# Kernel optimization log

Hardware: AMD Instinct MI355X
Metric: run time of the kernel (lower is better)

## Reference

```python
import jax, jax.numpy as jnp
import numpy as np
import math

RCR = 5.2
NUM_SPECIES = 7
AEV_DIM = 1008
WIDTHS = [1008, 256, 192, 160]


def setup_inputs() -> dict:
    key = jax.random.key(0)
    ks = jax.random.split(key, 12)
    B, N = 1, 2048
    species = jax.random.randint(ks[0], (B, N), 0, NUM_SPECIES, dtype=jnp.int64 if jax.config.read('jax_enable_x64') else jnp.int32)
    coordinates = jax.random.uniform(ks[1], (B, N, 3), dtype=jnp.float32) * 6.0
    EtaR = jnp.array([16.0], dtype=jnp.float32)
    ShfR = jnp.array([0.9 + 0.18 * x for x in range(16)], dtype=jnp.float32)
    s = 0.05
    W0 = jax.random.normal(ks[2], (NUM_SPECIES, WIDTHS[1], WIDTHS[0]), jnp.float32) * s
    b0 = jax.random.normal(ks[3], (NUM_SPECIES, WIDTHS[1]), jnp.float32) * s
    W1 = jax.random.normal(ks[4], (NUM_SPECIES, WIDTHS[2], WIDTHS[1]), jnp.float32) * s
    b1 = jax.random.normal(ks[5], (NUM_SPECIES, WIDTHS[2]), jnp.float32) * s
    W2 = jax.random.normal(ks[6], (NUM_SPECIES, WIDTHS[3], WIDTHS[2]), jnp.float32) * s
    b2 = jax.random.normal(ks[7], (NUM_SPECIES, WIDTHS[3]), jnp.float32) * s
    Wf = jax.random.normal(ks[8], (NUM_SPECIES, 1, WIDTHS[3]), jnp.float32) * s
    bf = jax.random.normal(ks[9], (NUM_SPECIES, 1), jnp.float32) * s
    return {'species': species, 'coordinates': coordinates, 'EtaR': EtaR, 'ShfR': ShfR,
            'W0': W0, 'b0': b0, 'W1': W1, 'b1': b1, 'W2': W2, 'b2': b2, 'Wf': Wf, 'bf': bf}


def _celu(x, alpha=0.1):
    return jnp.maximum(x, 0.0) + jnp.minimum(0.0, alpha * jnp.expm1(x / alpha))


def _aev(species, coordinates, EtaR, ShfR):
    B, N = species.shape
    diff = coordinates[:, :, None, :] - coordinates[:, None, :, :]  # [B,N,N,3]
    dsq = jnp.sum(diff * diff, axis=-1)
    safe = jnp.where(dsq > 0, dsq, 1.0)
    dist = jnp.sqrt(safe)  # [B,N,N], diag is a dummy 1.0
    mask = (dsq > 0) & (dist <= RCR)
    fc = (0.5 * jnp.cos(math.pi * dist / RCR) + 0.5) * mask.astype(jnp.float32)
    onehot = jax.nn.one_hot(species, NUM_SPECIES, dtype=jnp.float32)  # [B,N,S]
    core = jnp.exp(-EtaR[0] * (dist[..., None] - ShfR) ** 2)  # [B,N,N,R]
    weighted = core * fc[..., None]
    # sum over neighbor j, grouped by neighbor species s (species-major concat order)
    radial = jnp.einsum('bijr,bjs->bisr', weighted, onehot)  # [B,N,S,R]
    radial = radial.reshape(B, N, NUM_SPECIES * ShfR.shape[0])
    pad = AEV_DIM - radial.shape[-1]
    return jnp.pad(radial, ((0, 0), (0, 0), (0, pad)))


def reference(species, coordinates, EtaR, ShfR, W0, b0, W1, b1, W2, b2, Wf, bf):
    aev = _aev(species, coordinates, EtaR, ShfR)  # [B,N,1008]
    # run all 7 element nets on every atom (matches the module's redundant-compute semantics)
    h = _celu(jnp.einsum('soh,bnh->sbno', W0, aev) + b0[:, None, None, :])
    h = _celu(jnp.einsum('soh,sbnh->sbno', W1, h) + b1[:, None, None, :])
    h = _celu(jnp.einsum('soh,sbnh->sbno', W2, h) + b2[:, None, None, :])
    e = jnp.einsum('soh,sbnh->sbno', Wf, h) + bf[:, None, None, :]  # [S,B,N,1]
    onehot = jax.nn.one_hot(species, NUM_SPECIES, dtype=jnp.float32)  # [B,N,S]
    total = jnp.einsum('sbn,bns->', e[..., 0], onehot)
    return total.reshape(1)
```

## Files before the change

kernel.cpp:

```cpp
#include <hip/hip_runtime.h>

#define N_ATOMS 2048
#define NSPEC 7
#define NR 16
#define NFEAT 112
#define RCR_F 5.2f
#define H0 256
#define H1 192
#define H2 160
#define W0_PITCH 1008
#define TILE 8
#define NTILES (N_ATOMS / TILE)

#define WS_SEG     0
#define WS_SCOORD  16384
#define WS_AEV     65536

__device__ __forceinline__ float celu01(float x) {
    return x > 0.f ? x : 0.1f * (__expf(x * 10.f) - 1.f);
}

__global__ __launch_bounds__(256) void sort_kernel(const int* __restrict__ species,
                                                   const float* __restrict__ coords,
                                                   int* __restrict__ seg,
                                                   float4* __restrict__ scoord,
                                                   float* __restrict__ out) {
    __shared__ int cnt[NSPEC];
    __shared__ int cur[NSPEC];
    int t = threadIdx.x;
    if (t < NSPEC) cnt[t] = 0;
    __syncthreads();
    for (int a = t; a < N_ATOMS; a += 256) atomicAdd(&cnt[species[a]], 1);
    __syncthreads();
    if (t == 0) {
        int run = 0;
        for (int s = 0; s < NSPEC; s++) { seg[s] = run; cur[s] = run; run += cnt[s]; }
        seg[NSPEC] = run;
        out[0] = 0.0f;
    }
    __syncthreads();
    for (int a = t; a < N_ATOMS; a += 256) {
        int sp = species[a];
        int pos = atomicAdd(&cur[sp], 1);
        scoord[pos] = make_float4(coords[3*a], coords[3*a+1], coords[3*a+2], 0.f);
    }
}

__global__ __launch_bounds__(256) void aev_kernel(const float4* __restrict__ scoord,
                                                  const int* __restrict__ seg,
                                                  const float* __restrict__ ShfR,
                                                  const float* __restrict__ EtaR,
                                                  float* __restrict__ aev) {
    int s = blockIdx.y;
    int p = blockIdx.x * 4 + (threadIdx.x >> 6);
    int lane = threadIdx.x & 63;

    float4 ci = scoord[p];
    float eta = EtaR[0];
    float shf[NR];
#pragma unroll
    for (int r = 0; r < NR; r++) shf[r] = ShfR[r];
    float acc[NR];
#pragma unroll
    for (int r = 0; r < NR; r++) acc[r] = 0.f;

    int kbeg = seg[s] + lane;
    int kend = seg[s + 1];
    const float rc2 = RCR_F * RCR_F;
    const float cosk = 3.14159265358979f / RCR_F;

    for (int k = kbeg; k < kend; k += 64) {
        float4 cj = scoord[k];
        float dx = ci.x - cj.x, dy = ci.y - cj.y, dz = ci.z - cj.z;
        float dsq = dx*dx + dy*dy + dz*dz;
        bool valid = (dsq > 0.f) && (dsq <= rc2);
        float d = sqrtf(dsq);
        float fc = 0.5f * __cosf(d * cosk) + 0.5f;
        fc = valid ? fc : 0.f;
#pragma unroll
        for (int r = 0; r < NR; r++) {
            float u = d - shf[r];
            acc[r] = fmaf(__expf(-eta * u * u), fc, acc[r]);
        }
    }
#pragma unroll
    for (int r = 0; r < NR; r++) {
        float v = acc[r];
        v += __shfl_xor(v, 1);
        v += __shfl_xor(v, 2);
        v += __shfl_xor(v, 4);
        v += __shfl_xor(v, 8);
        v += __shfl_xor(v, 16);
        v += __shfl_xor(v, 32);
        acc[r] = v;
    }
    if (lane == 0) {
        float* dst = aev + (size_t)p * NFEAT + s * NR;
#pragma unroll
        for (int r = 0; r < NR; r += 4)
            *(float4*)(dst + r) = make_float4(acc[r], acc[r+1], acc[r+2], acc[r+3]);
    }
}

__global__ __launch_bounds__(512) void mlp_kernel(const float* __restrict__ aev,
                                                  const int* __restrict__ seg,
                                                  const float* __restrict__ W0,
                                                  const float* __restrict__ b0,
                                                  const float* __restrict__ W1,
                                                  const float* __restrict__ b1,
                                                  const float* __restrict__ W2,
                                                  const float* __restrict__ b2,
                                                  const float* __restrict__ Wf,
                                                  const float* __restrict__ bf,
                                                  float* __restrict__ out) {
    __shared__ float aevs[TILE][NFEAT];
    __shared__ float h0s[TILE][H0];
    __shared__ float h1s[TILE][H1];
    __shared__ float bsum;

    int s = blockIdx.y;
    int segend = seg[s + 1];
    int base = seg[s] + blockIdx.x * TILE;
    if (base >= segend) return;
    int n_act = min(TILE, segend - base);

    int t = threadIdx.x;
    if (t == 0) bsum = 0.f;

    {
        float4* dst = (float4*)&aevs[0][0];
        const float4* src = (const float4*)(aev + (size_t)base * NFEAT);
        int nfl4 = min(TILE * (NFEAT / 4), (N_ATOMS - base) * (NFEAT / 4));
        for (int j = t; j < TILE * (NFEAT / 4); j += 512)
            dst[j] = (j < nfl4) ? src[j] : make_float4(0.f, 0.f, 0.f, 0.f);
    }
    __syncthreads();

    int o = t >> 1, ks = t & 1;

    {
        const float* Wr = W0 + (size_t)(s * H0 + o) * W0_PITCH + ks * 4;
        float bias = b0[s * H0 + o];
        float acc[TILE];
#pragma unroll
        for (int q = 0; q < TILE; q++) acc[q] = 0.f;
#pragma unroll 7
        for (int i = 0; i < NFEAT / 8; i++) {
            float4 w = *(const float4*)(Wr + i * 8);
#pragma unroll
            for (int q = 0; q < TILE; q++) {
                float4 a = *(const float4*)(&aevs[q][i * 8 + ks * 4]);
                acc[q] += w.x*a.x + w.y*a.y + w.z*a.z + w.w*a.w;
            }
        }
#pragma unroll
        for (int q = 0; q < TILE; q++) {
            float v = acc[q];
            v += __shfl_xor(v, 1);
            if (ks == 0) h0s[q][o] = celu01(v + bias);
        }
    }
    __syncthreads();

    if (o < H1) {
        const float* Wr = W1 + (size_t)(s * H1 + o) * H0 + ks * 4;
        float bias = b1[s * H1 + o];
        float acc[TILE];
#pragma unroll
        for (int q = 0; q < TILE; q++) acc[q] = 0.f;
#pragma unroll 4
        for (int i = 0; i < H0 / 8; i++) {
            float4 w = *(const float4*)(Wr + i * 8);
#pragma unroll
            for (int q = 0; q < TILE; q++) {
                float4 a = *(const float4*)(&h0s[q][i * 8 + ks * 4]);
                acc[q] += w.x*a.x + w.y*a.y + w.z*a.z + w.w*a.w;
            }
        }
#pragma unroll
        for (int q = 0; q < TILE; q++) {
            float v = acc[q];
            v += __shfl_xor(v, 1);
            if (ks == 0) h1s[q][o] = celu01(v + bias);
        }
    }
    __syncthreads();

    float contrib = 0.f;
    if (o < H2) {
        const float* Wr = W2 + (size_t)(s * H2 + o) * H1 + ks * 4;
        float bias = b2[s * H2 + o];
        float wf = Wf[s * H2 + o];
        float acc[TILE];
#pragma unroll
        for (int q = 0; q < TILE; q++) acc[q] = 0.f;
#pragma unroll 4
        for (int i = 0; i < H1 / 8; i++) {
            float4 w = *(const float4*)(Wr + i * 8);
#pragma unroll
            for (int q = 0; q < TILE; q++) {
                float4 a = *(const float4*)(&h1s[q][i * 8 + ks * 4]);
                acc[q] += w.x*a.x + w.y*a.y + w.z*a.z + w.w*a.w;
            }
        }
#pragma unroll
        for (int q = 0; q < TILE; q++) {
            float v = acc[q];
            v += __shfl_xor(v, 1);
            if (ks == 0 && q < n_act) contrib += wf * celu01(v + bias);
        }
    }
    if (t == 0) contrib += (float)n_act * bf[s];

    float v = contrib;
    v += __shfl_down(v, 32);
    v += __shfl_down(v, 16);
    v += __shfl_down(v, 8);
    v += __shfl_down(v, 4);
    v += __shfl_down(v, 2);
    v += __shfl_down(v, 1);
    if ((t & 63) == 0) atomicAdd(&bsum, v);
    __syncthreads();
    if (t == 0) atomicAdd(out, bsum);
}

extern "C" void kernel_launch(void* const* d_in, const int* in_sizes, int n_in,
                              void* d_out, int out_size, void* d_ws, size_t ws_size,
                              hipStream_t stream) {
    const int*   species = (const int*)d_in[0];
    const float* coords  = (const float*)d_in[1];
    const float* EtaR    = (const float*)d_in[2];
    const float* ShfR    = (const float*)d_in[3];
    const float* W0      = (const float*)d_in[4];
    const float* b0      = (const float*)d_in[5];
    const float* W1      = (const float*)d_in[6];
    const float* b1      = (const float*)d_in[7];
    const float* W2      = (const float*)d_in[8];
    const float* b2      = (const float*)d_in[9];
    const float* Wf      = (const float*)d_in[10];
    const float* bf      = (const float*)d_in[11];
    float* out = (float*)d_out;
    char* ws = (char*)d_ws;

    int*    seg    = (int*)(ws + WS_SEG);
    float4* scoord = (float4*)(ws + WS_SCOORD);
    float*  aev    = (float*)(ws + WS_AEV);

    hipLaunchKernelGGL(sort_kernel, dim3(1), dim3(256), 0, stream,
                       species, coords, seg, scoord, out);
    hipLaunchKernelGGL(aev_kernel, dim3(N_ATOMS / 4, NSPEC), dim3(256), 0, stream,
                       scoord, seg, ShfR, EtaR, aev);
    hipLaunchKernelGGL(mlp_kernel, dim3(NTILES, NSPEC), dim3(512), 0, stream,
                       aev, seg, W0, b0, W1, b1, W2, b2, Wf, bf, out);
}
```

Measured before the change: 154.7 us.

## Split MLP into per-layer bf16 MFMA kernels with pre-converted weights

Replaces the fused fp32 FMA MLP kernel with three per-layer kernels that use 16x16x32 bf16 MFMA instructions. A prep kernel converts the weights to bf16 with padding on every call, and the AEV kernel now writes bf16 activations. Per-tile partial sums go to a buffer, and a final reduce kernel sums them and adds the bias terms, removing the global atomics. The cost is more kernel launches, hidden activations written to and read back from global memory, a per-call weight conversion pass, and reduced precision.

```diff
diff --git a/kernel.cpp b/kernel.cpp
--- a/kernel.cpp
+++ b/kernel.cpp
@@ -4,20 +4,37 @@
 #define NSPEC 7
 #define NR 16
 #define NFEAT 112
+#define K0P 128
 #define RCR_F 5.2f
 #define H0 256
 #define H1 192
 #define H2 160
 #define W0_PITCH 1008
-#define TILE 8
-#define NTILES (N_ATOMS / TILE)
+#define NTILE16 128
+#define GY2 (H2 / 16)
+#define NPART (NSPEC * GY2 * NTILE16)
+
+typedef __attribute__((ext_vector_type(8))) short short8;
+typedef __attribute__((ext_vector_type(4))) float floatx4;
 
 #define WS_SEG     0
 #define WS_SCOORD  16384
-#define WS_AEV     65536
+#define WS_AEVB    65536
+#define WS_H0B     655360
+#define WS_H1B     1769472
+#define WS_WB0     2621440
+#define WS_WB1     3145728
+#define WS_WB2     3866624
+#define WS_PART    4325376
 
 __device__ __forceinline__ float celu01(float x) {
     return x > 0.f ? x : 0.1f * (__expf(x * 10.f) - 1.f);
+}
+
+__device__ __forceinline__ unsigned short f2bf(float x) {
+    unsigned int u = __float_as_uint(x);
+    u = (u + 0x7FFFu + ((u >> 16) & 1u)) >> 16;
+    return (unsigned short)u;
 }
 
 __global__ __launch_bounds__(256) void sort_kernel(const int* __restrict__ species,
@@ -46,11 +63,34 @@
     }
 }
 
+#define S0E (NSPEC * H0 * K0P)
+#define S1E (NSPEC * H1 * H0)
+#define S2E (NSPEC * H2 * H1)
+__global__ __launch_bounds__(256) void prep_kernel(const float* __restrict__ W0,
+                                                   const float* __restrict__ W1,
+                                                   const float* __restrict__ W2,
+                                                   unsigned short* __restrict__ wb0,
+                                                   unsigned short* __restrict__ wb1,
+                                                   unsigned short* __restrict__ wb2) {
+    int idx = blockIdx.x * 256 + threadIdx.x;
+    if (idx < S0E) {
+        int k = idx & 127, r = idx >> 7;
+        float v = (k < NFEAT) ? W0[(size_t)r * W0_PITCH + k] : 0.f;
+        wb0[idx] = f2bf(v);
+    } else if (idx < S0E + S1E) {
+        int j = idx - S0E;
+        wb1[j] = f2bf(W1[j]);
+    } else if (idx < S0E + S1E + S2E) {
+        int j = idx - S0E - S1E;
+        wb2[j] = f2bf(W2[j]);
+    }
+}
+
 __global__ __launch_bounds__(256) void aev_kernel(const float4* __restrict__ scoord,
                                                   const int* __restrict__ seg,
                                                   const float* __restrict__ ShfR,
                                                   const float* __restrict__ EtaR,
-                                                  float* __restrict__ aev) {
+                                                  unsigned short* __restrict__ aevb) {
     int s = blockIdx.y;
     int p = blockIdx.x * 4 + (threadIdx.x >> 6);
     int lane = threadIdx.x & 63;
@@ -95,133 +135,117 @@
         acc[r] = v;
     }
     if (lane == 0) {
-        float* dst = aev + (size_t)p * NFEAT + s * NR;
-#pragma unroll
-        for (int r = 0; r < NR; r += 4)
-            *(float4*)(dst + r) = make_float4(acc[r], acc[r+1], acc[r+2], acc[r+3]);
-    }
-}
-
-__global__ __launch_bounds__(512) void mlp_kernel(const float* __restrict__ aev,
-                                                  const int* __restrict__ seg,
-                                                  const float* __restrict__ W0,
-                                                  const float* __restrict__ b0,
-                                                  const float* __restrict__ W1,
-                                                  const float* __restrict__ b1,
-                                                  const float* __restrict__ W2,
-                                                  const float* __restrict__ b2,
-                                                  const float* __restrict__ Wf,
-                                                  const float* __restrict__ bf,
-                                                  float* __restrict__ out) {
-    __shared__ float aevs[TILE][NFEAT];
-    __shared__ float h0s[TILE][H0];
-    __shared__ float h1s[TILE][H1];
-    __shared__ float bsum;
-
-    int s = blockIdx.y;
+        unsigned short* dst = aevb + (size_t)p * K0P + s * NR;
+#pragma unroll
+        for (int r = 0; r < NR; r++) dst[r] = f2bf(acc[r]);
+        if (s == 0) {
+            unsigned short* pz = aevb + (size_t)p * K0P + NFEAT;
+#pragma unroll
+            for (int r = 0; r < K0P - NFEAT; r++) pz[r] = 0;
+        }
+    }
+}
+
+template<int KSTEPS, int KP, int NTOT, int NPOUT>
+__global__ __launch_bounds__(64) void mfma_layer(const unsigned short* __restrict__ act,
+                                                 const unsigned short* __restrict__ wb,
+                                                 const float* __restrict__ bias,
+                                                 const int* __restrict__ seg,
+                                                 unsigned short* __restrict__ outbuf) {
+    int s = blockIdx.z;
     int segend = seg[s + 1];
-    int base = seg[s] + blockIdx.x * TILE;
+    int base = seg[s] + blockIdx.x * 16;
     if (base >= segend) return;
-    int n_act = min(TILE, segend - base);
-
+    int nbase = blockIdx.y * 16;
+
+    int lane = threadIdx.x;
+    int r = lane & 15, quad = lane >> 4;
+
+    const unsigned short* arow = act + (size_t)(base + r) * KP + quad * 8;
+    const unsigned short* brow = wb + ((size_t)(s * NTOT + nbase + r)) * KP + quad * 8;
+
+    floatx4 acc = {0.f, 0.f, 0.f, 0.f};
+#pragma unroll
+    for (int ks = 0; ks < KSTEPS; ks++) {
+        short8 a = *(const short8*)(arow + ks * 32);
+        short8 b = *(const short8*)(brow + ks * 32);
+        acc = __builtin_amdgcn_mfma_f32_16x16x32_bf16(a, b, acc, 0, 0, 0);
+    }
+    float bi = bias[s * NTOT + nbase + r];
+#pragma unroll
+    for (int reg = 0; reg < 4; reg++) {
+        int atom = base + quad * 4 + reg;
+        if (atom < segend)
+            outbuf[(size_t)atom * NPOUT + nbase + r] = f2bf(celu01(acc[reg] + bi));
+    }
+}
+
+__global__ __launch_bounds__(64) void mfma_final(const unsigned short* __restrict__ act,
+                                                 const unsigned short* __restrict__ wb,
+                                                 const float* __restrict__ bias,
+                                                 const float* __restrict__ Wf,
+                                                 const int* __restrict__ seg,
+                                                 float* __restrict__ part) {
+    int s = blockIdx.z;
+    int pidx = (s * GY2 + blockIdx.y) * NTILE16 + blockIdx.x;
+    int segend = seg[s + 1];
+    int base = seg[s] + blockIdx.x * 16;
+    int lane = threadIdx.x;
+    if (base >= segend) {
+        if (lane == 0) part[pidx] = 0.f;
+        return;
+    }
+    int nbase = blockIdx.y * 16;
+    int r = lane & 15, quad = lane >> 4;
+
+    const unsigned short* arow = act + (size_t)(base + r) * H1 + quad * 8;
+    const unsigned short* brow = wb + ((size_t)(s * H2 + nbase + r)) * H1 + quad * 8;
+
+    floatx4 acc = {0.f, 0.f, 0.f, 0.f};
+#pragma unroll
+    for (int ks = 0; ks < H1 / 32; ks++) {
+        short8 a = *(const short8*)(arow + ks * 32);
+        short8 b = *(const short8*)(brow + ks * 32);
+        acc = __builtin_amdgcn_mfma_f32_16x16x32_bf16(a, b, acc, 0, 0, 0);
+    }
+    float bi = bias[s * H2 + nbase + r];
+    float wf = Wf[s * H2 + nbase + r];
+    float e = 0.f;
+#pragma unroll
+    for (int reg = 0; reg < 4; reg++) {
+        int atom = base + quad * 4 + reg;
+        if (atom < segend) e += wf * celu01(acc[reg] + bi);
+    }
+    e += __shfl_xor(e, 1);
+    e += __shfl_xor(e, 2);
+    e += __shfl_xor(e, 4);
+    e += __shfl_xor(e, 8);
+    e += __shfl_xor(e, 16);
+    e += __shfl_xor(e, 32);
+    if (lane == 0) part[pidx] = e;
+}
+
+__global__ __launch_bounds__(256) void reduce_kernel(const float* __restrict__ part,
+                                                     const int* __restrict__ seg,
+                                                     const float* __restrict__ bf,
+                                                     float* __restrict__ out) {
+    __shared__ float wsum[4];
     int t = threadIdx.x;
-    if (t == 0) bsum = 0.f;
-
-    {
-        float4* dst = (float4*)&aevs[0][0];
-        const float4* src = (const float4*)(aev + (size_t)base * NFEAT);
-        int nfl4 = min(TILE * (NFEAT / 4), (N_ATOMS - base) * (NFEAT / 4));
-        for (int j = t; j < TILE * (NFEAT / 4); j += 512)
-            dst[j] = (j < nfl4) ? src[j] : make_float4(0.f, 0.f, 0.f, 0.f);
-    }
-    __syncthreads();
-
-    int o = t >> 1, ks = t & 1;
-
-    {
-        const float* Wr = W0 + (size_t)(s * H0 + o) * W0_PITCH + ks * 4;
-        float bias = b0[s * H0 + o];
-        float acc[TILE];
-#pragma unroll
-        for (int q = 0; q < TILE; q++) acc[q] = 0.f;
-#pragma unroll 7
-        for (int i = 0; i < NFEAT / 8; i++) {
-            float4 w = *(const float4*)(Wr + i * 8);
-#pragma unroll
-            for (int q = 0; q < TILE; q++) {
-                float4 a = *(const float4*)(&aevs[q][i * 8 + ks * 4]);
-                acc[q] += w.x*a.x + w.y*a.y + w.z*a.z + w.w*a.w;
-            }
-        }
-#pragma unroll
-        for (int q = 0; q < TILE; q++) {
-            float v = acc[q];
-            v += __shfl_xor(v, 1);
-            if (ks == 0) h0s[q][o] = celu01(v + bias);
-        }
-    }
-    __syncthreads();
-
-    if (o < H1) {
-        const float* Wr = W1 + (size_t)(s * H1 + o) * H0 + ks * 4;
-        float bias = b1[s * H1 + o];
-        float acc[TILE];
-#pragma unroll
-        for (int q = 0; q < TILE; q++) acc[q] = 0.f;
-#pragma unroll 4
-        for (int i = 0; i < H0 / 8; i++) {
-            float4 w = *(const float4*)(Wr + i * 8);
-#pragma unroll
-            for (int q = 0; q < TILE; q++) {
-                float4 a = *(const float4*)(&h0s[q][i * 8 + ks * 4]);
-                acc[q] += w.x*a.x + w.y*a.y + w.z*a.z + w.w*a.w;
-            }
-        }
-#pragma unroll
-        for (int q = 0; q < TILE; q++) {
-            float v = acc[q];
-            v += __shfl_xor(v, 1);
-            if (ks == 0) h1s[q][o] = celu01(v + bias);
-        }
-    }
-    __syncthreads();
-
-    float contrib = 0.f;
-    if (o < H2) {
-        const float* Wr = W2 + (size_t)(s * H2 + o) * H1 + ks * 4;
-        float bias = b2[s * H2 + o];
-        float wf = Wf[s * H2 + o];
-        float acc[TILE];
-#pragma unroll
-        for (int q = 0; q < TILE; q++) acc[q] = 0.f;
-#pragma unroll 4
-        for (int i = 0; i < H1 / 8; i++) {
-            float4 w = *(const float4*)(Wr + i * 8);
-#pragma unroll
-            for (int q = 0; q < TILE; q++) {
-                float4 a = *(const float4*)(&h1s[q][i * 8 + ks * 4]);
-                acc[q] += w.x*a.x + w.y*a.y + w.z*a.z + w.w*a.w;
-            }
-        }
-#pragma unroll
-        for (int q = 0; q < TILE; q++) {
-            float v = acc[q];
-            v += __shfl_xor(v, 1);
-            if (ks == 0 && q < n_act) contrib += wf * celu01(v + bias);
-        }
-    }
-    if (t == 0) contrib += (float)n_act * bf[s];
-
-    float v = contrib;
+    float v = 0.f;
+    for (int i = t; i < NPART; i += 256) v += part[i];
     v += __shfl_down(v, 32);
     v += __shfl_down(v, 16);
     v += __shfl_down(v, 8);
     v += __shfl_down(v, 4);
     v += __shfl_down(v, 2);
     v += __shfl_down(v, 1);
-    if ((t & 63) == 0) atomicAdd(&bsum, v);
-    __syncthreads();
-    if (t == 0) atomicAdd(out, bsum);
+    if ((t & 63) == 0) wsum[t >> 6] = v;
+    __syncthreads();
+    if (t == 0) {
+        float tot = wsum[0] + wsum[1] + wsum[2] + wsum[3];
+        for (int s = 0; s < NSPEC; s++) tot += (float)(seg[s + 1] - seg[s]) * bf[s];
+        out[0] = tot;
+    }
 }
 
 extern "C" void kernel_launch(void* const* d_in, const int* in_sizes, int n_in,
@@ -242,14 +266,28 @@
     float* out = (float*)d_out;
     char* ws = (char*)d_ws;
 
-    int*    seg    = (int*)(ws + WS_SEG);
-    float4* scoord = (float4*)(ws + WS_SCOORD);
-    float*  aev    = (float*)(ws + WS_AEV);
+    int*            seg    = (int*)(ws + WS_SEG);
+    float4*         scoord = (float4*)(ws + WS_SCOORD);
+    unsigned short* aevb   = (unsigned short*)(ws + WS_AEVB);
+    unsigned short* h0b    = (unsigned short*)(ws + WS_H0B);
+    unsigned short* h1b    = (unsigned short*)(ws + WS_H1B);
+    unsigned short* wb0    = (unsigned short*)(ws + WS_WB0);
+    unsigned short* wb1    = (unsigned short*)(ws + WS_WB1);
+    unsigned short* wb2    = (unsigned short*)(ws + WS_WB2);
+    float*          part   = (float*)(ws + WS_PART);
 
     hipLaunchKernelGGL(sort_kernel, dim3(1), dim3(256), 0, stream,
                        species, coords, seg, scoord, out);
+    hipLaunchKernelGGL(prep_kernel, dim3((S0E + S1E + S2E + 255) / 256), dim3(256), 0, stream,
+                       W0, W1, W2, wb0, wb1, wb2);
     hipLaunchKernelGGL(aev_kernel, dim3(N_ATOMS / 4, NSPEC), dim3(256), 0, stream,
-                       scoord, seg, ShfR, EtaR, aev);
-    hipLaunchKernelGGL(mlp_kernel, dim3(NTILES, NSPEC), dim3(512), 0, stream,
-                       aev, seg, W0, b0, W1, b1, W2, b2, Wf, bf, out);
-}
+                       scoord, seg, ShfR, EtaR, aevb);
+    hipLaunchKernelGGL((mfma_layer<K0P / 32, K0P, H0, H0>), dim3(NTILE16, H0 / 16, NSPEC),
+                       dim3(64), 0, stream, aevb, wb0, b0, seg, h0b);
+    hipLaunchKernelGGL((mfma_layer<H0 / 32, H0, H1, H1>), dim3(NTILE16, H1 / 16, NSPEC),
+                       dim3(64), 0, stream, h0b, wb1, b1, seg, h1b);
+    hipLaunchKernelGGL(mfma_final, dim3(NTILE16, GY2, NSPEC), dim3(64), 0, stream,
+                       h1b, wb2, b2, Wf, seg, part);
+    hipLaunchKernelGGL(reduce_kernel, dim3(1), dim3(256), 0, stream,
+                       part, seg, bf, out);
+}
```

Measured after the change: 157.3 us. About the same (+1.7%).
